# Kernel tuning notes

Measured on AMD Instinct MI355X. Metric: run time of the kernel, lower is better.

The kernel has to match this reference:

```python
import jax, jax.numpy as jnp
import numpy as np

H, KV, HD, HID = 32, 8, 128, 4096
THETA, FACTOR, HI_FF, LO_FF, ORIG_MAX = 500000.0, 8.0, 4.0, 1.0, 8192


def _llama3_inv_freq():
    # standard Llama-3 rope scaling
    inv = 1.0 / (THETA ** (np.arange(0, HD, 2, dtype=np.float64) / HD))
    wavelen = 2.0 * np.pi / inv
    low_wl = ORIG_MAX / LO_FF
    high_wl = ORIG_MAX / HI_FF
    smooth = (ORIG_MAX / wavelen - LO_FF) / (HI_FF - LO_FF)
    scaled = np.where(wavelen > low_wl, inv / FACTOR, inv)
    mid = (wavelen <= low_wl) & (wavelen >= high_wl)
    scaled = np.where(mid, (1 - smooth) * inv / FACTOR + smooth * inv, scaled)
    return scaled.astype(np.float32)


def _rope_cos_sin(T):
    inv = _llama3_inv_freq()                       # [HD/2]
    pos = np.arange(T, dtype=np.float32)
    freqs = pos[:, None] * inv[None, :]            # [T, HD/2]
    emb = np.concatenate([freqs, freqs], axis=-1)  # [T, HD]
    return jnp.asarray(np.cos(emb)), jnp.asarray(np.sin(emb))


def _rotate_half(x):
    x1, x2 = jnp.split(x, 2, axis=-1)
    return jnp.concatenate([-x2, x1], axis=-1)


def setup_inputs() -> dict:
    key = jax.random.key(0)
    ks = jax.random.split(key, 5)
    s = 1.0 / np.sqrt(HID)
    return {
        "x": jax.random.normal(ks[0], (1, 2048, HID), jnp.float32),
        "wq": jax.random.normal(ks[1], (HID, H * HD), jnp.float32) * s,
        "wk": jax.random.normal(ks[2], (HID, KV * HD), jnp.float32) * s,
        "wv": jax.random.normal(ks[3], (HID, KV * HD), jnp.float32) * s,
        "wo": jax.random.normal(ks[4], (H * HD, HID), jnp.float32) * s,
    }


def reference(x, wq, wk, wv, wo):
    B, T, _ = x.shape
    q = (x @ wq).reshape(B, T, H, HD).transpose(0, 2, 1, 3)   # [B,H,T,D]
    k = (x @ wk).reshape(B, T, KV, HD).transpose(0, 2, 1, 3)  # [B,KV,T,D]
    v = (x @ wv).reshape(B, T, KV, HD).transpose(0, 2, 1, 3)
    cos, sin = _rope_cos_sin(T)                               # [T,D]
    q = q * cos + _rotate_half(q) * sin
    k = k * cos + _rotate_half(k) * sin
    rep = H // KV
    k = jnp.repeat(k, rep, axis=1)                            # [B,H,T,D]
    v = jnp.repeat(v, rep, axis=1)
    scores = jnp.einsum("bhtd,bhsd->bhts", q, k) * (1.0 / np.sqrt(HD))
    mask = jnp.tril(jnp.ones((T, T), dtype=bool))
    scores = jnp.where(mask, scores, -jnp.inf)
    att = jax.nn.softmax(scores, axis=-1)
    out = jnp.einsum("bhts,bhsd->bhtd", att, v)
    out = out.transpose(0, 2, 1, 3).reshape(B, T, H * HD)
    return out @ wo
```

## Files before the change

kernel.cpp:

```cpp
#include <hip/hip_runtime.h>
#include <math.h>

#define T_SEQ 2048
#define HID   4096
#define NH    32
#define NKV   8
#define HD    128
#define QCOLS (NH*HD)
#define KCOLS (NKV*HD)
#define KSTR  2048

typedef _Float16 f16;
typedef _Float16 f16x8 __attribute__((ext_vector_type(8)));
typedef _Float16 f16x4 __attribute__((ext_vector_type(4)));
typedef float f32x4 __attribute__((ext_vector_type(4)));

#define GLDS(g, l) __builtin_amdgcn_global_load_lds( \
    (const __attribute__((address_space(1))) void*)(g), \
    (__attribute__((address_space(3))) void*)(l), 16, 0, 0)

__global__ void rope_table(float* __restrict__ cosT, float* __restrict__ sinT) {
    int idx = blockIdx.x * blockDim.x + threadIdx.x;
    if (idx >= T_SEQ * 64) return;
    int t = idx >> 6, i = idx & 63;
    double inv = pow(500000.0, -(double)(2 * i) / 128.0);
    double wavelen = 6.283185307179586 / inv;
    const double lowwl = 8192.0, highwl = 2048.0;
    double scaled;
    if (wavelen > lowwl) {
        scaled = inv / 8.0;
    } else if (wavelen >= highwl) {
        double smooth = (8192.0 / wavelen - 1.0) / 3.0;
        scaled = (1.0 - smooth) * inv / 8.0 + smooth * inv;
    } else {
        scaled = inv;
    }
    float invf = (float)scaled;
    float phase = (float)t * invf;
    cosT[idx] = (float)cos((double)phase);
    sinT[idx] = (float)sin((double)phase);
}

__global__ void convert_f32_f16(const float* __restrict__ in, f16* __restrict__ out, int n8) {
    int i = blockIdx.x * blockDim.x + threadIdx.x;
    if (i >= n8) return;
    float4 a = *(const float4*)(in + (size_t)i * 8);
    float4 b = *(const float4*)(in + (size_t)i * 8 + 4);
    f16x8 v = {(f16)a.x, (f16)a.y, (f16)a.z, (f16)a.w, (f16)b.x, (f16)b.y, (f16)b.z, (f16)b.w};
    *(f16x8*)(out + (size_t)i * 8) = v;
}

__global__ __launch_bounds__(256) void transpose_f32_to_f16(const float* __restrict__ in,
                                                            f16* __restrict__ out,
                                                            int R, int ld) {
    __shared__ f16 t[64][72];
    const int tid = threadIdx.x;
    const int r0 = blockIdx.y * 64, c0 = blockIdx.x * 64;
#pragma unroll
    for (int i = 0; i < 4; ++i) {
        int r = i * 16 + (tid >> 4), c4 = (tid & 15) * 4;
        float4 v = *(const float4*)(in + (size_t)(r0 + r) * ld + c0 + c4);
        t[r][c4 + 0] = (f16)v.x; t[r][c4 + 1] = (f16)v.y;
        t[r][c4 + 2] = (f16)v.z; t[r][c4 + 3] = (f16)v.w;
    }
    __syncthreads();
    int n = tid >> 2, j0 = (tid & 3) * 16;
    f16x8 a, b;
#pragma unroll
    for (int j = 0; j < 8; ++j) { a[j] = t[j0 + j][n]; b[j] = t[j0 + 8 + j][n]; }
    *(f16x8*)(out + (size_t)(c0 + n) * R + r0 + j0) = a;
    *(f16x8*)(out + (size_t)(c0 + n) * R + r0 + j0 + 8) = b;
}

__global__ __launch_bounds__(256) void transpose_f16(const f16* __restrict__ in,
                                                     f16* __restrict__ out,
                                                     int R, int ld) {
    __shared__ f16 t[64][72];
    const int tid = threadIdx.x;
    const int r0 = blockIdx.y * 64, c0 = blockIdx.x * 64;
#pragma unroll
    for (int i = 0; i < 2; ++i) {
        int r = i * 32 + (tid >> 3), c8 = (tid & 7) * 8;
        f16x8 v = *(const f16x8*)(in + (size_t)(r0 + r) * ld + c0 + c8);
#pragma unroll
        for (int j = 0; j < 8; ++j) t[r][c8 + j] = v[j];
    }
    __syncthreads();
    int n = tid >> 2, j0 = (tid & 3) * 16;
    f16x8 a, b;
#pragma unroll
    for (int j = 0; j < 8; ++j) { a[j] = t[j0 + j][n]; b[j] = t[j0 + 8 + j][n]; }
    *(f16x8*)(out + (size_t)(c0 + n) * R + r0 + j0) = a;
    *(f16x8*)(out + (size_t)(c0 + n) * R + r0 + j0 + 8) = b;
}

template <typename OutT>
__global__ __launch_bounds__(256, 2) void gemm_f16(const f16* __restrict__ A,
                                                   const f16* __restrict__ Bt,
                                                   OutT* __restrict__ C,
                                                   int M, int ldc, int K) {
    __shared__ f16 As[2][128 * 64];
    __shared__ f16 Bs[2][128 * 64];
    const int tid = threadIdx.x;
    const int l = tid & 63;
    const int w = tid >> 6, wr = w >> 1, wc = w & 1;
    const int c16 = l & 15, g = l >> 4;
    const int m0 = blockIdx.y * 128, n0 = blockIdx.x * 128;

    f32x4 acc[4][4] = {};

    const int r_src = tid >> 3;
    const int colswz = ((tid & 7) * 8) ^ ((r_src & 7) << 3);
    const f16* gA = A + (size_t)(m0 + r_src) * K + colswz;
    const f16* gB = Bt + (size_t)(n0 + r_src) * K + colswz;

    auto stage = [&](f16* sA, f16* sB, int k0) {
#pragma unroll
        for (int i = 0; i < 4; ++i) {
            GLDS(gA + (size_t)(i * 32) * K + k0, sA + i * 2048 + tid * 8);
            GLDS(gB + (size_t)(i * 32) * K + k0, sB + i * 2048 + tid * 8);
        }
    };
    auto compute = [&](const f16* sA, const f16* sB) {
#pragma unroll
        for (int kk = 0; kk < 2; ++kk) {
            f16x8 af[4], bf[4];
#pragma unroll
            for (int mb = 0; mb < 4; ++mb) {
                int row = wr * 64 + mb * 16 + c16;
                af[mb] = *(const f16x8*)((const char*)sA + row * 128 +
                                         ((kk * 64 + g * 16) ^ ((row & 7) << 4)));
            }
#pragma unroll
            for (int nb = 0; nb < 4; ++nb) {
                int row = wc * 64 + nb * 16 + c16;
                bf[nb] = *(const f16x8*)((const char*)sB + row * 128 +
                                         ((kk * 64 + g * 16) ^ ((row & 7) << 4)));
            }
#pragma unroll
            for (int mb = 0; mb < 4; ++mb)
#pragma unroll
                for (int nb = 0; nb < 4; ++nb)
                    acc[mb][nb] = __builtin_amdgcn_mfma_f32_16x16x32_f16(af[mb], bf[nb], acc[mb][nb], 0, 0, 0);
        }
    };

    stage(As[0], Bs[0], 0);
    __syncthreads();
    int cur = 0;
    for (int k0 = 64; k0 < K; k0 += 64) {
        stage(As[cur ^ 1], Bs[cur ^ 1], k0);
        compute(As[cur], Bs[cur]);
        __syncthreads();
        cur ^= 1;
    }
    compute(As[cur], Bs[cur]);

#pragma unroll
    for (int mb = 0; mb < 4; ++mb)
#pragma unroll
        for (int nb = 0; nb < 4; ++nb)
#pragma unroll
            for (int r = 0; r < 4; ++r) {
                size_t row = m0 + wr * 64 + mb * 16 + g * 4 + r;
                C[row * ldc + n0 + wc * 64 + nb * 16 + c16] = (OutT)acc[mb][nb][r];
            }
}

__global__ void rope_apply_f16(f16* __restrict__ data, const float* __restrict__ cosT,
                               const float* __restrict__ sinT, int nheads, int stride) {
    int idx = blockIdx.x * blockDim.x + threadIdx.x;
    int lane = idx & 63;
    int row = idx >> 6;
    if (row >= T_SEQ * nheads) return;
    int t = row / nheads, h = row % nheads;
    f16* p = data + (size_t)t * stride + h * HD;
    float c = cosT[t * 64 + lane], s = sinT[t * 64 + lane];
    float x1 = (float)p[lane], x2 = (float)p[lane + 64];
    p[lane]      = (f16)(x1 * c - x2 * s);
    p[lane + 64] = (f16)(x2 * c + x1 * s);
}

__global__ __launch_bounds__(256, 3) void attn_f16(const f16* __restrict__ q,
                                                   const f16* __restrict__ k,
                                                   const f16* __restrict__ vt,
                                                   f16* __restrict__ outh) {
    __shared__ f16 Ks[64 * 128];
    __shared__ f16 Vs[128 * 64];
    __shared__ f16 Ps[4][16 * 72];
    const int tid = threadIdx.x;
    const int l = tid & 63, w = tid >> 6;
    const int c16 = l & 15, g = l >> 4;
    const int h = blockIdx.y, kvh = h >> 2;
    const float SCALE = 0.08838834764831845f;

    const int kr = tid >> 4, kboff = (tid & 15) * 16;
    const int vr = tid >> 3, vboff = (tid & 7) * 16;
    const char* kgb = (const char*)(k + kvh * HD);
    const char* vgb = (const char*)(vt + (size_t)(kvh * HD) * T_SEQ);

    for (int pass = 0; pass < 2; ++pass) {
        const int qt = pass ? 31 - (int)blockIdx.x : (int)blockIdx.x;
        const int qrow = qt * 64 + w * 16 + c16;

        f16x8 qf[4];
        const f16* qbase = q + (size_t)qrow * QCOLS + h * HD;
#pragma unroll
        for (int ks = 0; ks < 4; ++ks) qf[ks] = *(const f16x8*)(qbase + ks * 32 + g * 8);

        f32x4 o[8] = {};
        float mrun = -INFINITY, lrun = 0.f;

        for (int ch = 0; ch <= qt; ++ch) {
            __syncthreads();
#pragma unroll
            for (int i = 0; i < 4; ++i) {
                int r = i * 16 + kr;
                GLDS(kgb + (size_t)(ch * 64 + r) * (KSTR * 2) + (kboff ^ ((r & 7) << 4)),
                     (char*)Ks + i * 4096 + tid * 16);
                int d = i * 32 + vr;
                GLDS(vgb + (size_t)d * (T_SEQ * 2) + (size_t)(ch * 64) * 2 + (vboff ^ ((d & 7) << 4)),
                     (char*)Vs + i * 4096 + tid * 16);
            }
            __syncthreads();

            f32x4 st[4];
            __builtin_amdgcn_s_setprio(1);
#pragma unroll
            for (int kb = 0; kb < 4; ++kb) {
                f32x4 a = {};
#pragma unroll
                for (int ks = 0; ks < 4; ++ks) {
                    int row = kb * 16 + c16;
                    f16x8 kf = *(const f16x8*)((const char*)Ks + row * 256 +
                                               ((ks * 64 + g * 16) ^ ((row & 7) << 4)));
                    a = __builtin_amdgcn_mfma_f32_16x16x32_f16(kf, qf[ks], a, 0, 0, 0);
                }
                st[kb] = a;
            }
            __builtin_amdgcn_s_setprio(0);

            float p[16];
            float cmax = -INFINITY;
            const bool diag = (ch == qt);
#pragma unroll
            for (int kb = 0; kb < 4; ++kb)
#pragma unroll
                for (int r = 0; r < 4; ++r) {
                    float s = st[kb][r] * SCALE;
                    if (diag) {
                        int key = ch * 64 + kb * 16 + g * 4 + r;
                        if (key > qrow) s = -INFINITY;
                    }
                    p[kb * 4 + r] = s;
                    cmax = fmaxf(cmax, s);
                }
            cmax = fmaxf(cmax, __shfl_xor(cmax, 16));
            cmax = fmaxf(cmax, __shfl_xor(cmax, 32));
            float mnew = fmaxf(mrun, cmax);
            float corr = __expf(mrun - mnew);
            float psum = 0.f;
#pragma unroll
            for (int i = 0; i < 16; ++i) { float e = __expf(p[i] - mnew); p[i] = e; psum += e; }
            psum += __shfl_xor(psum, 16);
            psum += __shfl_xor(psum, 32);
            lrun = lrun * corr + psum;
            mrun = mnew;
#pragma unroll
            for (int mb = 0; mb < 8; ++mb) o[mb] *= corr;

            f16* pw = Ps[w] + c16 * 72;
#pragma unroll
            for (int kb = 0; kb < 4; ++kb) {
                f16x4 q4 = {(f16)p[kb * 4], (f16)p[kb * 4 + 1], (f16)p[kb * 4 + 2], (f16)p[kb * 4 + 3]};
                *(f16x4*)(pw + kb * 16 + g * 4) = q4;
            }

            __builtin_amdgcn_s_setprio(1);
#pragma unroll
            for (int ks2 = 0; ks2 < 2; ++ks2) {
                f16x8 pf = *(const f16x8*)(Ps[w] + c16 * 72 + ks2 * 32 + g * 8);
#pragma unroll
                for (int mb = 0; mb < 8; ++mb) {
                    int row = mb * 16 + c16;
                    f16x8 vf = *(const f16x8*)((const char*)Vs + row * 128 +
                                               ((ks2 * 64 + g * 16) ^ ((row & 7) << 4)));
                    o[mb] = __builtin_amdgcn_mfma_f32_16x16x32_f16(vf, pf, o[mb], 0, 0, 0);
                }
            }
            __builtin_amdgcn_s_setprio(0);
        }

        float invl = 1.f / lrun;
        f16* ob = outh + (size_t)qrow * QCOLS + h * HD;
#pragma unroll
        for (int mb = 0; mb < 8; ++mb) {
            f16x4 v = {(f16)(o[mb][0] * invl), (f16)(o[mb][1] * invl),
                       (f16)(o[mb][2] * invl), (f16)(o[mb][3] * invl)};
            *(f16x4*)(ob + mb * 16 + g * 4) = v;
        }
    }
}

extern "C" void kernel_launch(void* const* d_in, const int* in_sizes, int n_in,
                              void* d_out, int out_size, void* d_ws, size_t ws_size,
                              hipStream_t stream) {
    const float* x  = (const float*)d_in[0];
    const float* wq = (const float*)d_in[1];
    const float* wk = (const float*)d_in[2];
    const float* wv = (const float*)d_in[3];
    const float* wo = (const float*)d_in[4];
    float* out = (float*)d_out;

    char* ws = (char*)d_ws;
    const size_t MB = 1024ULL * 1024ULL;
    float* cosT = (float*)(ws);
    float* sinT = (float*)(ws + 512 * 1024ULL);
    f16* xh   = (f16*)(ws + 1 * MB);
    f16* atth = xh;
    f16* qh   = (f16*)(ws + 17 * MB);
    f16* kvh  = (f16*)(ws + 33 * MB);
    f16* wT   = (f16*)(ws + 41 * MB);
    f16* vtb  = (f16*)(ws + 73 * MB);

    rope_table<<<dim3((T_SEQ * 64 + 255) / 256), dim3(256), 0, stream>>>(cosT, sinT);
    convert_f32_f16<<<dim3(T_SEQ * HID / 8 / 256), dim3(256), 0, stream>>>(x, xh, T_SEQ * HID / 8);

    transpose_f32_to_f16<<<dim3(QCOLS / 64, HID / 64), dim3(256), 0, stream>>>(wq, wT, HID, QCOLS);
    gemm_f16<f16><<<dim3(QCOLS / 128, T_SEQ / 128), dim3(256), 0, stream>>>(
        xh, wT, qh, T_SEQ, QCOLS, HID);

    transpose_f32_to_f16<<<dim3(KCOLS / 64, HID / 64), dim3(256), 0, stream>>>(wk, wT, HID, KCOLS);
    transpose_f32_to_f16<<<dim3(KCOLS / 64, HID / 64), dim3(256), 0, stream>>>(
        wv, wT + (size_t)KCOLS * HID, HID, KCOLS);
    gemm_f16<f16><<<dim3(KSTR / 128, T_SEQ / 128), dim3(256), 0, stream>>>(
        xh, wT, kvh, T_SEQ, KSTR, HID);

    rope_apply_f16<<<dim3(T_SEQ * NH * 64 / 256), dim3(256), 0, stream>>>(
        qh, cosT, sinT, NH, QCOLS);
    rope_apply_f16<<<dim3(T_SEQ * NKV * 64 / 256), dim3(256), 0, stream>>>(
        kvh, cosT, sinT, NKV, KSTR);

    transpose_f16<<<dim3(KCOLS / 64, T_SEQ / 64), dim3(256), 0, stream>>>(
        kvh + KCOLS, vtb, T_SEQ, KSTR);

    attn_f16<<<dim3(16, NH), dim3(256), 0, stream>>>(qh, kvh, vtb, atth);

    transpose_f32_to_f16<<<dim3(HID / 64, QCOLS / 64), dim3(256), 0, stream>>>(wo, wT, QCOLS, HID);
    gemm_f16<float><<<dim3(HID / 128, T_SEQ / 128), dim3(256), 0, stream>>>(
        atth, wT, out, T_SEQ, HID, QCOLS);
}
```

Before: 357.4 us.

## Double-buffer K/V tiles, fuse Q RoPE into attention, lazy softmax rescale

```diff
diff --git a/kernel.cpp b/kernel.cpp
--- a/kernel.cpp
+++ b/kernel.cpp
@@ -181,12 +181,14 @@
     p[lane + 64] = (f16)(x2 * c + x1 * s);
 }
 
-__global__ __launch_bounds__(256, 3) void attn_f16(const f16* __restrict__ q,
+__global__ __launch_bounds__(256, 2) void attn_f16(const f16* __restrict__ q,
                                                    const f16* __restrict__ k,
                                                    const f16* __restrict__ vt,
+                                                   const float* __restrict__ cosT,
+                                                   const float* __restrict__ sinT,
                                                    f16* __restrict__ outh) {
-    __shared__ f16 Ks[64 * 128];
-    __shared__ f16 Vs[128 * 64];
+    __shared__ f16 Ks[2][64 * 128];
+    __shared__ f16 Vs[2][128 * 64];
     __shared__ f16 Ps[4][16 * 72];
     const int tid = threadIdx.x;
     const int l = tid & 63, w = tid >> 6;
@@ -199,30 +201,56 @@
     const char* kgb = (const char*)(k + kvh * HD);
     const char* vgb = (const char*)(vt + (size_t)(kvh * HD) * T_SEQ);
 
+    auto stage = [&](int buf, int ch) {
+#pragma unroll
+        for (int i = 0; i < 4; ++i) {
+            int r = i * 16 + kr;
+            GLDS(kgb + (size_t)(ch * 64 + r) * (KSTR * 2) + (kboff ^ ((r & 7) << 4)),
+                 (char*)Ks[buf] + i * 4096 + tid * 16);
+            int d = i * 32 + vr;
+            GLDS(vgb + (size_t)d * (T_SEQ * 2) + (size_t)(ch * 64) * 2 + (vboff ^ ((d & 7) << 4)),
+                 (char*)Vs[buf] + i * 4096 + tid * 16);
+        }
+    };
+
     for (int pass = 0; pass < 2; ++pass) {
         const int qt = pass ? 31 - (int)blockIdx.x : (int)blockIdx.x;
         const int qrow = qt * 64 + w * 16 + c16;
 
         f16x8 qf[4];
-        const f16* qbase = q + (size_t)qrow * QCOLS + h * HD;
-#pragma unroll
-        for (int ks = 0; ks < 4; ++ks) qf[ks] = *(const f16x8*)(qbase + ks * 32 + g * 8);
+        {
+            const f16* qbase = q + (size_t)qrow * QCOLS + h * HD;
+            f16x8 qraw[4];
+#pragma unroll
+            for (int ks = 0; ks < 4; ++ks) qraw[ks] = *(const f16x8*)(qbase + ks * 32 + g * 8);
+            const float* cb = cosT + qrow * 64;
+            const float* sb = sinT + qrow * 64;
+#pragma unroll
+            for (int ks = 0; ks < 2; ++ks) {
+                int dbase = ks * 32 + g * 8;
+                float4 c0 = *(const float4*)(cb + dbase);
+                float4 c1 = *(const float4*)(cb + dbase + 4);
+                float4 s0 = *(const float4*)(sb + dbase);
+                float4 s1 = *(const float4*)(sb + dbase + 4);
+                float cA[8] = {c0.x, c0.y, c0.z, c0.w, c1.x, c1.y, c1.z, c1.w};
+                float sA[8] = {s0.x, s0.y, s0.z, s0.w, s1.x, s1.y, s1.z, s1.w};
+#pragma unroll
+                for (int j = 0; j < 8; ++j) {
+                    float lo = (float)qraw[ks][j], hi = (float)qraw[ks + 2][j];
+                    qf[ks][j]     = (f16)(lo * cA[j] - hi * sA[j]);
+                    qf[ks + 2][j] = (f16)(hi * cA[j] + lo * sA[j]);
+                }
+            }
+        }
 
         f32x4 o[8] = {};
         float mrun = -INFINITY, lrun = 0.f;
 
+        stage(0, 0);
+        __syncthreads();
+        int cur = 0;
         for (int ch = 0; ch <= qt; ++ch) {
-            __syncthreads();
-#pragma unroll
-            for (int i = 0; i < 4; ++i) {
-                int r = i * 16 + kr;
-                GLDS(kgb + (size_t)(ch * 64 + r) * (KSTR * 2) + (kboff ^ ((r & 7) << 4)),
-                     (char*)Ks + i * 4096 + tid * 16);
-                int d = i * 32 + vr;
-                GLDS(vgb + (size_t)d * (T_SEQ * 2) + (size_t)(ch * 64) * 2 + (vboff ^ ((d & 7) << 4)),
-                     (char*)Vs + i * 4096 + tid * 16);
-            }
-            __syncthreads();
+            if (ch < qt) stage(cur ^ 1, ch + 1);
 
             f32x4 st[4];
             __builtin_amdgcn_s_setprio(1);
@@ -232,7 +260,7 @@
 #pragma unroll
                 for (int ks = 0; ks < 4; ++ks) {
                     int row = kb * 16 + c16;
-                    f16x8 kf = *(const f16x8*)((const char*)Ks + row * 256 +
+                    f16x8 kf = *(const f16x8*)((const char*)Ks[cur] + row * 256 +
                                                ((ks * 64 + g * 16) ^ ((row & 7) << 4)));
                     a = __builtin_amdgcn_mfma_f32_16x16x32_f16(kf, qf[ks], a, 0, 0, 0);
                 }
@@ -257,17 +285,25 @@
                 }
             cmax = fmaxf(cmax, __shfl_xor(cmax, 16));
             cmax = fmaxf(cmax, __shfl_xor(cmax, 32));
-            float mnew = fmaxf(mrun, cmax);
-            float corr = __expf(mrun - mnew);
+
+            float muse;
+            if (__all(cmax <= mrun + 8.f)) {
+                muse = mrun;
+            } else {
+                float mnew = fmaxf(mrun, cmax);
+                float corr = __expf(mrun - mnew);
+                lrun *= corr;
+#pragma unroll
+                for (int mb = 0; mb < 8; ++mb) o[mb] *= corr;
+                mrun = mnew;
+                muse = mnew;
+            }
             float psum = 0.f;
 #pragma unroll
-            for (int i = 0; i < 16; ++i) { float e = __expf(p[i] - mnew); p[i] = e; psum += e; }
+            for (int i = 0; i < 16; ++i) { float e = __expf(p[i] - muse); p[i] = e; psum += e; }
             psum += __shfl_xor(psum, 16);
             psum += __shfl_xor(psum, 32);
-            lrun = lrun * corr + psum;
-            mrun = mnew;
-#pragma unroll
-            for (int mb = 0; mb < 8; ++mb) o[mb] *= corr;
+            lrun += psum;
 
             f16* pw = Ps[w] + c16 * 72;
 #pragma unroll
@@ -283,12 +319,15 @@
 #pragma unroll
                 for (int mb = 0; mb < 8; ++mb) {
                     int row = mb * 16 + c16;
-                    f16x8 vf = *(const f16x8*)((const char*)Vs + row * 128 +
+                    f16x8 vf = *(const f16x8*)((const char*)Vs[cur] + row * 128 +
                                                ((ks2 * 64 + g * 16) ^ ((row & 7) << 4)));
                     o[mb] = __builtin_amdgcn_mfma_f32_16x16x32_f16(vf, pf, o[mb], 0, 0, 0);
                 }
             }
             __builtin_amdgcn_s_setprio(0);
+
+            __syncthreads();
+            cur ^= 1;
         }
 
         float invl = 1.f / lrun;
@@ -336,15 +375,13 @@
     gemm_f16<f16><<<dim3(KSTR / 128, T_SEQ / 128), dim3(256), 0, stream>>>(
         xh, wT, kvh, T_SEQ, KSTR, HID);
 
-    rope_apply_f16<<<dim3(T_SEQ * NH * 64 / 256), dim3(256), 0, stream>>>(
-        qh, cosT, sinT, NH, QCOLS);
     rope_apply_f16<<<dim3(T_SEQ * NKV * 64 / 256), dim3(256), 0, stream>>>(
         kvh, cosT, sinT, NKV, KSTR);
 
     transpose_f16<<<dim3(KCOLS / 64, T_SEQ / 64), dim3(256), 0, stream>>>(
         kvh + KCOLS, vtb, T_SEQ, KSTR);
 
-    attn_f16<<<dim3(16, NH), dim3(256), 0, stream>>>(qh, kvh, vtb, atth);
+    attn_f16<<<dim3(16, NH), dim3(256), 0, stream>>>(qh, kvh, vtb, cosT, sinT, atth);
 
     transpose_f32_to_f16<<<dim3(HID / 64, QCOLS / 64), dim3(256), 0, stream>>>(wo, wT, QCOLS, HID);
     gemm_f16<float><<<dim3(HID / 128, T_SEQ / 128), dim3(256), 0, stream>>>(
```

New measurement: 350.7 us. About the same (-1.9%).
